# Kernel optimization log

Measured on AMD Instinct MI355X. Metric: run time of the kernel, lower is better.

The kernel has to match this reference:

```python
import jax, jax.numpy as jnp
import numpy as np

B, P, C = 32, 8732, 21
TOP_K = 200
CONF_THRESH = 0.01
NMS_THRESH = 0.45
VAR0, VAR1 = 0.1, 0.2  # VOC PRIOR_BOX VARIANCE


def setup_inputs() -> dict:
    key = jax.random.key(0)
    k1, k2, k3 = jax.random.split(key, 3)
    loc_data = jax.random.normal(k1, (B, P, 4), jnp.float32)
    conf_data = jax.random.uniform(k2, (B, P, C), jnp.float32)
    prior_data = jax.random.uniform(k3, (P, 4), jnp.float32)
    return {"loc_data": loc_data, "conf_data": conf_data, "prior_data": prior_data}


def _decode(loc, priors):
    # priors are (cx, cy, w, h); returns (x1, y1, x2, y2)
    cxcy = priors[:, :2] + loc[:, :2] * VAR0 * priors[:, 2:]
    wh = priors[:, 2:] * jnp.exp(loc[:, 2:] * VAR1)
    x1y1 = cxcy - wh * 0.5
    return jnp.concatenate([x1y1, x1y1 + wh], axis=1)  # [P,4]


def _nms_class(boxes, scores):
    # boxes [P,4], scores [P] -> [TOP_K,5] rows of (score, x1, y1, x2, y2)
    s = jnp.where(scores > CONF_THRESH, scores, -1.0)
    top_s, idx = jax.lax.top_k(s, TOP_K)          # descending scores
    b = boxes[idx]                                 # [K,4]
    valid = top_s > CONF_THRESH
    x1, y1, x2, y2 = b[:, 0], b[:, 1], b[:, 2], b[:, 3]
    area = (x2 - x1) * (y2 - y1)
    # pairwise intersection / IoU [K,K]
    xx1 = jnp.maximum(x1[:, None], x1[None, :])
    yy1 = jnp.maximum(y1[:, None], y1[None, :])
    xx2 = jnp.minimum(x2[:, None], x2[None, :])
    yy2 = jnp.minimum(y2[:, None], y2[None, :])
    inter = jnp.clip(xx2 - xx1, 0.0) * jnp.clip(yy2 - yy1, 0.0)
    union = area[:, None] + area[None, :] - inter
    iou = inter / union
    ar = jnp.arange(TOP_K)

    def step(carry, j):
        kept, suppressed = carry
        is_kept = valid[j] & ~suppressed[j]
        kept = kept.at[j].set(is_kept)
        suppressed = suppressed | (is_kept & (iou[j] > NMS_THRESH) & (ar > j))
        return (kept, suppressed), None

    (kept, _), _ = jax.lax.scan(
        step, (jnp.zeros(TOP_K, bool), jnp.zeros(TOP_K, bool)), ar)
    # compact kept rows to the front (matches output[i, cl, :count] = ...)
    pos = jnp.cumsum(kept) - 1
    safe = jnp.where(kept, pos, TOP_K)
    rows = jnp.concatenate([top_s[:, None], b], axis=1)  # [K,5]
    out = jnp.zeros((TOP_K + 1, 5), rows.dtype).at[safe].set(rows)[:TOP_K]
    return out


def reference(loc_data, conf_data, prior_data):
    def per_image(loc, conf):
        boxes = _decode(loc, prior_data)           # [P,4]
        return jax.vmap(lambda s: _nms_class(boxes, s), in_axes=1)(conf)  # [C,K,5]

    out = jax.vmap(per_image)(loc_data, conf_data)  # [B,C,K,5]
    return out.at[:, 0].set(0.0)  # class 0 (background) is skipped in original
```

## Files before the change

### kernel.cpp

```cpp
#include <hip/hip_runtime.h>
#include <stdint.h>

#define B_ 32
#define P_ 8732
#define C_ 21
#define TOPK 200
#define TGT 228
#define TGT0 300
#define SUBCAP 28
#define NCH2 35
#define NSLOT (NCH2 * SUBCAP)
#define CONF_T 0.01f
#define NMS_T 0.45f
#define NT 512
#define KV4 5
#define NTASK (B_ * C_)

__device__ __forceinline__ uint32_t f2s(float f) {
    uint32_t u = __float_as_uint(f);
    return (u & 0x80000000u) ? ~u : (u | 0x80000000u);
}
__device__ __forceinline__ float s2f(uint32_t s) {
    uint32_t b = (s & 0x80000000u) ? (s & 0x7FFFFFFFu) : ~s;
    return __uint_as_float(b);
}
__device__ __forceinline__ uint32_t keyof(float v) {
    return f2s((v > CONF_T) ? v : -1.0f);
}
__device__ __forceinline__ uint32_t thr0() {
    return f2s(1.0f - (float)TGT0 / (float)P_);
}

__global__ __launch_bounds__(256) void scatter_cands(const float* __restrict__ conf,
                                                     uint32_t* __restrict__ gccnt,
                                                     uint64_t* __restrict__ gcand) {
    const int b = blockIdx.x / NCH2;
    const int ch = blockIdx.x % NCH2;
    const int p0 = ch * 256;
    const int n = min(256, P_ - p0);
    const int tid = threadIdx.x;
    const int lane = tid & 63;
    const int cs = tid >> 6;
    __shared__ float tile[256 * C_];
    const float4* src4 = (const float4*)(conf + ((size_t)b * P_ + p0) * C_);
    float4* tile4 = (float4*)tile;
    const int tot4 = (n * C_) >> 2;
    for (int i = tid; i < tot4; i += 256) tile4[i] = src4[i];
    __syncthreads();
    const uint32_t T0 = thr0();
    const bool act = (4 * lane) < n;
    for (int c = (cs == 0 ? 4 : cs); c < C_; c += 4) {
        uint32_t kk[4];
        int nq = 0;
        if (act) {
            const float* tp = &tile[4 * lane * C_ + c];
            kk[0] = keyof(tp[0 * C_]);
            kk[1] = keyof(tp[1 * C_]);
            kk[2] = keyof(tp[2 * C_]);
            kk[3] = keyof(tp[3 * C_]);
            nq = (kk[0] >= T0) + (kk[1] >= T0) + (kk[2] >= T0) + (kk[3] >= T0);
        }
        int incl = nq;
        #pragma unroll
        for (int d = 1; d < 64; d <<= 1) {
            int v = __shfl_up(incl, d);
            if (lane >= d) incl += v;
        }
        const int excl = incl - nq;
        const int total = __shfl(incl, 63);
        const int task = b * C_ + c;
        uint64_t* dst = gcand + ((size_t)task * NCH2 + ch) * SUBCAP;
        if (nq) {
            int pos = excl;
            const int pb = p0 + 4 * lane;
            #pragma unroll
            for (int k = 0; k < 4; ++k) {
                if (kk[k] >= T0) {
                    if (pos < SUBCAP)
                        dst[pos] = ((uint64_t)kk[k] << 32) | (uint32_t)(~(uint32_t)(pb + k));
                    ++pos;
                }
            }
        }
        if (lane == 0) gccnt[(size_t)task * NCH2 + ch] = (uint32_t)total;
    }
}

template<bool HASWS>
__global__ __launch_bounds__(NT, 6) void detect_kernel(
    const float* __restrict__ loc, const float* __restrict__ prior,
    const uint32_t* __restrict__ gccnt, const uint64_t* __restrict__ gcand,
    const float* __restrict__ conf, float* __restrict__ out)
{
    const int task = blockIdx.x;
    const int b = task / C_;
    const int c = task % C_;
    const int tid = threadIdx.x;
    const int lane = tid & 63;
    float* outp = out + (size_t)task * TOPK * 5;

    if (c == 0) {
        for (int e = tid; e < TOPK * 5; e += NT) outp[e] = 0.0f;
        return;
    }

    __shared__ uint64_t cand[256];
    __shared__ float4 bbox[TOPK];
    __shared__ float bs[TOPK];
    __shared__ unsigned long long msk[TOPK * 4];
    __shared__ unsigned long long vmask[4];
    __shared__ int order[TOPK];
    __shared__ int s_cnt, s_nk;
    __shared__ int s_c2[2];
    __shared__ uint32_t s_ccnt[NCH2];
    __shared__ int s_gc, s_bad;

    const uint32_t T0 = thr0();

    if (tid == 0) s_cnt = 0;
    if (tid < 2) s_c2[tid] = 0;
    if (HASWS && tid < NCH2) s_ccnt[tid] = gccnt[(size_t)task * NCH2 + tid];
    for (int i2 = tid; i2 < TOPK * 4; i2 += NT) msk[i2] = 0ull;
    __syncthreads();
    if (HASWS && tid < 64) {
        uint32_t cc = (lane < NCH2) ? s_ccnt[lane] : 0u;
        int bad = (cc > SUBCAP) ? 1 : 0;
        int tot = (int)cc;
        #pragma unroll
        for (int d = 1; d < 64; d <<= 1) {
            tot += __shfl_down(tot, d);
            bad |= __shfl_down(bad, d);
        }
        if (lane == 0) { s_gc = tot; s_bad = bad; }
    }
    __syncthreads();

    const bool fast = HASWS && !s_bad && s_gc >= TOPK;
    const int gc = HASWS ? s_gc : 0;

    uint64_t vc0 = 0, vc1 = 0;
    bool val0 = false, val1 = false;
    uint4 kv[KV4];
    if (fast) {
        const uint64_t* gp = gcand + (size_t)task * NSLOT;
        {
            const int ch0 = tid / SUBCAP, i0 = tid - ch0 * SUBCAP;
            if (i0 < (int)s_ccnt[ch0]) { vc0 = gp[tid]; val0 = true; }
        }
        const int s1 = tid + NT;
        if (s1 < NSLOT) {
            const int ch1 = s1 / SUBCAP, i1 = s1 - ch1 * SUBCAP;
            if (i1 < (int)s_ccnt[ch1]) { vc1 = gp[s1]; val1 = true; }
        }
    } else {
        const float* sp = conf + (size_t)b * P_ * C_ + c;
        #pragma unroll
        for (int r = 0; r < KV4; ++r) {
            uint32_t uu[4];
            #pragma unroll
            for (int c4 = 0; c4 < 4; ++c4) {
                int p = (tid + r * NT) * 4 + c4;
                if (p < P_) {
                    float v = sp[(size_t)p * C_];
                    v = (v > CONF_T) ? v : -1.0f;
                    uu[c4] = f2s(v);
                } else uu[c4] = 0u;
            }
            kv[r] = make_uint4(uu[0], uu[1], uu[2], uu[3]);
        }
    }

    if (fast) {
        uint32_t vthr = T0;
        if (gc > 256) {
            const uint32_t k0 = (uint32_t)(vc0 >> 32);
            const uint32_t k1 = (uint32_t)(vc1 >> 32);
            uint32_t lo = T0, hi = 0xFFFFFFFFu;
            uint32_t t;
            {
                const float sc = s2f(T0);
                const float sn = 1.0f - (1.0f - sc) * (float)TGT / (float)gc;
                t = f2s(sn);
                if (!(t > lo && t < hi)) t = lo + ((hi - lo) >> 1);
            }
            for (int it = 0; ; ++it) {
                const int slot = it & 1;
                int my = (val0 && k0 >= t) + (val1 && k1 >= t);
                #pragma unroll
                for (int d = 1; d < 64; d <<= 1) my += __shfl_down(my, d);
                if (lane == 0) atomicAdd(&s_c2[slot], my);
                __syncthreads();
                const int cnt = s_c2[slot];
                __syncthreads();
                if (tid == 0) s_c2[slot] = 0;
                if (cnt >= TOPK && cnt <= 256) { vthr = t; break; }
                if (cnt > 256) lo = t; else hi = t;
                if (hi - lo <= 1) { vthr = lo; break; }
                uint32_t tn = 0;
                bool bis = (it >= 8) || (cnt == 0);
                if (!bis) {
                    const float sc = s2f(t);
                    const float sn = 1.0f - (1.0f - sc) * (float)TGT / (float)cnt;
                    tn = f2s(sn);
                    if (!(tn > lo && tn < hi)) bis = true;
                }
                if (bis) tn = lo + ((hi - lo) >> 1);
                t = tn;
            }
        }
        if (val0 && (uint32_t)(vc0 >> 32) >= vthr) {
            int pos = atomicAdd(&s_cnt, 1);
            if (pos < 256) cand[pos] = vc0;
        }
        if (val1 && (uint32_t)(vc1 >> 32) >= vthr) {
            int pos = atomicAdd(&s_cnt, 1);
            if (pos < 256) cand[pos] = vc1;
        }
    } else {
        uint32_t lo = 0u, hi = 0xFFFFFFFFu;
        uint32_t t = f2s(1.0f - (float)TGT / (float)P_);
        uint32_t vthr = 0u;
        for (int it = 0; ; ++it) {
            const int slot = it & 1;
            int my = 0;
            #pragma unroll
            for (int r = 0; r < KV4; ++r)
                my += (kv[r].x >= t) + (kv[r].y >= t) + (kv[r].z >= t) + (kv[r].w >= t);
            #pragma unroll
            for (int d = 1; d < 64; d <<= 1) my += __shfl_down(my, d);
            if (lane == 0) atomicAdd(&s_c2[slot], my);
            __syncthreads();
            const int cnt = s_c2[slot];
            __syncthreads();
            if (tid == 0) s_c2[slot] = 0;
            if (cnt >= TOPK && cnt <= 256) { vthr = t; break; }
            if (cnt > 256) lo = t; else hi = t;
            if (hi - lo <= 1) { vthr = lo; break; }
            uint32_t tn = 0;
            bool bis = (it >= 8) || (cnt == 0);
            if (!bis) {
                const float sc = s2f(t);
                const float sn = 1.0f - (1.0f - sc) * (float)TGT / (float)cnt;
                tn = f2s(sn);
                if (!(tn > lo && tn < hi)) bis = true;
            }
            if (bis) tn = lo + ((hi - lo) >> 1);
            t = tn;
        }
        #pragma unroll
        for (int r = 0; r < KV4; ++r) {
            const int pb = (tid + r * NT) * 4;
            uint32_t uu[4] = {kv[r].x, kv[r].y, kv[r].z, kv[r].w};
            #pragma unroll
            for (int c4 = 0; c4 < 4; ++c4) {
                uint32_t u = uu[c4];
                if (u >= vthr) {
                    int pos = atomicAdd(&s_cnt, 1);
                    if (pos < 256) cand[pos] = ((uint64_t)u << 32) | (uint32_t)(~(uint32_t)(pb + c4));
                }
            }
        }
    }
    __syncthreads();
    if (tid < 256 && tid >= s_cnt) cand[tid] = 0ull;
    __syncthreads();

    uint64_t v = (tid < 256) ? cand[tid] : 0ull;
    for (int kk = 2; kk <= 256; kk <<= 1) {
        for (int j = kk >> 1; j > 0; j >>= 1) {
            if (j >= 64) {
                __syncthreads();
                if (tid < 256) cand[tid] = v;
                __syncthreads();
                if (tid < 256) {
                    uint64_t pv = cand[tid ^ j];
                    bool keepmax = (((tid & j) == 0) == ((tid & kk) == 0));
                    v = keepmax ? (v > pv ? v : pv) : (v < pv ? v : pv);
                }
            } else if (tid < 256) {
                uint64_t pv = __shfl_xor(v, j);
                bool keepmax = (((tid & j) == 0) == ((tid & kk) == 0));
                v = keepmax ? (v > pv ? v : pv) : (v < pv ? v : pv);
            }
        }
    }

    float my_sc = -1.0f;
    if (tid < TOPK) {
        uint32_t su = (uint32_t)(v >> 32);
        int p = (int)(~(uint32_t)v);
        my_sc = s2f(su);
        const float4 l4 = *(const float4*)(loc + ((size_t)b * P_ + p) * 4);
        const float4 pr = *(const float4*)(prior + (size_t)p * 4);
        float cx = __fadd_rn(pr.x, __fmul_rn(__fmul_rn(l4.x, 0.1f), pr.z));
        float cy = __fadd_rn(pr.y, __fmul_rn(__fmul_rn(l4.y, 0.1f), pr.w));
        float ew = (float)exp((double)__fmul_rn(l4.z, 0.2f));
        float eh = (float)exp((double)__fmul_rn(l4.w, 0.2f));
        float w  = __fmul_rn(pr.z, ew);
        float h  = __fmul_rn(pr.w, eh);
        float x1 = __fsub_rn(cx, __fmul_rn(w, 0.5f));
        float y1 = __fsub_rn(cy, __fmul_rn(h, 0.5f));
        float x2 = __fadd_rn(x1, w);
        float y2 = __fadd_rn(y1, h);
        bs[tid] = my_sc;
        bbox[tid] = make_float4(x1, y1, x2, y2);
    }
    {
        unsigned long long bm = __ballot(tid < TOPK && my_sc > CONF_T);
        if (lane == 0 && tid < 256) vmask[tid >> 6] = bm;
    }
    __syncthreads();

    if (tid < 500) {
        const int rp = tid / 5;
        const int s  = tid - rp * 5;
        #pragma unroll
        for (int pass = 0; pass < 2; ++pass) {
            const int j  = pass ? (199 - rp) : rp;
            const int i0 = j + 1 + s;
            const float4 bj = bbox[j];
            const float  aj = __fmul_rn(__fsub_rn(bj.z, bj.x), __fsub_rn(bj.w, bj.y));
            for (int i = i0; i < TOPK; i += 5) {
                const float4 bi = bbox[i];
                float xx1 = fmaxf(bj.x, bi.x);
                float yy1 = fmaxf(bj.y, bi.y);
                float xx2 = fminf(bj.z, bi.z);
                float yy2 = fminf(bj.w, bi.w);
                float dx = fmaxf(__fsub_rn(xx2, xx1), 0.0f);
                float dy = fmaxf(__fsub_rn(yy2, yy1), 0.0f);
                float inter = __fmul_rn(dx, dy);
                if (inter > 0.0f) {
                    float ai = __fmul_rn(__fsub_rn(bi.z, bi.x), __fsub_rn(bi.w, bi.y));
                    float uni = __fsub_rn(__fadd_rn(aj, ai), inter);
                    float t45 = __fmul_rn(NMS_T, uni);
                    float mar = __fmul_rn(t45, 1e-6f);
                    bool sup;
                    if (inter > __fadd_rn(t45, mar)) sup = true;
                    else if (inter < __fsub_rn(t45, mar)) sup = false;
                    else sup = (inter / uni > NMS_T);
                    if (sup) atomicOr(&msk[j * 4 + (i >> 6)], 1ull << (i & 63));
                }
            }
        }
    }
    __syncthreads();

    if (tid < 64) {
        const int L = tid;
        auto or_reduce = [&](unsigned long long x) {
            #pragma unroll
            for (int d = 1; d < 64; d <<= 1) x |= __shfl_xor(x, d);
            return x;
        };
        unsigned long long s1 = 0, s2 = 0, s3 = 0;
        int nk = 0;
        #pragma unroll
        for (int w = 0; w < 4; ++w) {
            const int j = (w << 6) | L;
            unsigned long long r0 = 0, r1 = 0, r2 = 0, r3 = 0;
            if (j < TOPK) {
                const unsigned long long* mr = &msk[j * 4];
                r0 = mr[0]; r1 = mr[1]; r2 = mr[2]; r3 = mr[3];
            }
            const unsigned long long rself = (w == 0) ? r0 : (w == 1) ? r1
                                           : (w == 2) ? r2 : r3;
            unsigned long long sw = (w == 0) ? 0ull : (w == 1) ? s1
                                  : (w == 2) ? s2 : s3;
            unsigned long long alive = vmask[w] & ~sw;
            unsigned long long pm = 0;
            while (alive) {
                int jl = __ffsll(alive) - 1;
                if (L == 0) order[nk] = (w << 6) | jl;
                ++nk;
                sw |= __shfl(rself, jl);
                pm |= (1ull << jl);
                alive &= ~(sw | (1ull << jl));
            }
            if (pm) {
                const bool picked = (pm >> L) & 1ull;
                if (w == 0) {
                    s1 |= or_reduce(picked ? r1 : 0ull);
                    s2 |= or_reduce(picked ? r2 : 0ull);
                    s3 |= or_reduce(picked ? r3 : 0ull);
                } else if (w == 1) {
                    s2 |= or_reduce(picked ? r2 : 0ull);
                    s3 |= or_reduce(picked ? r3 : 0ull);
                } else if (w == 2) {
                    s3 |= or_reduce(picked ? r3 : 0ull);
                }
            }
        }
        if (L == 0) s_nk = nk;
    }
    __syncthreads();

    const int nk = s_nk;
    for (int e = tid; e < TOPK * 5; e += NT) {
        int r = e / 5;
        int f = e - r * 5;
        float val = 0.0f;
        if (r < nk) {
            int j = order[r];
            float4 bb = bbox[j];
            val = (f == 0) ? bs[j] : (f == 1) ? bb.x : (f == 2) ? bb.y
                : (f == 3) ? bb.z : bb.w;
        }
        outp[e] = val;
    }
}

extern "C" void kernel_launch(void* const* d_in, const int* in_sizes, int n_in,
                              void* d_out, int out_size, void* d_ws, size_t ws_size,
                              hipStream_t stream) {
    const float* loc   = (const float*)d_in[0];
    const float* conf  = (const float*)d_in[1];
    const float* prior = (const float*)d_in[2];
    float* out = (float*)d_out;

    const size_t cnt_bytes  = (size_t)NTASK * NCH2 * sizeof(uint32_t);
    const size_t cand_bytes = (size_t)NTASK * NSLOT * sizeof(uint64_t);
    if (ws_size >= cnt_bytes + cand_bytes) {
        uint32_t* gccnt = (uint32_t*)d_ws;
        uint64_t* gcand = (uint64_t*)((char*)d_ws + cnt_bytes);
        scatter_cands<<<B_ * NCH2, 256, 0, stream>>>(conf, gccnt, gcand);
        detect_kernel<true><<<NTASK, NT, 0, stream>>>(loc, prior, gccnt, gcand, conf, out);
    } else {
        detect_kernel<false><<<NTASK, NT, 0, stream>>>(loc, prior, nullptr, nullptr, conf, out);
    }
}
```

Before: 123.0 us.

## Use ballot-based compaction, triple-buffer bisection counters, precompute box areas

In the scatter kernel, each lane now handles strided rows (lane+64k), and output positions come from per-k ballots and popcounts instead of a shuffle-up prefix scan. In the detect kernel's fast path, the threshold bisection rotates through three shared counter slots so one __syncthreads per iteration can be removed, and candidates are appended with one wave-level atomic instead of one atomic per thread. Box areas are computed once into shared memory, and the IoU inner loop is unrolled by two. These target shuffle-scan latency, barrier count, and LDS atomic contention. The candidate order inside each chunk changes, and the three-slot reset scheme depends on subtle reuse timing to stay correct.

```diff
diff --git a/kernel.cpp b/kernel.cpp
--- a/kernel.cpp
+++ b/kernel.cpp
@@ -48,37 +48,34 @@
     for (int i = tid; i < tot4; i += 256) tile4[i] = src4[i];
     __syncthreads();
     const uint32_t T0 = thr0();
-    const bool act = (4 * lane) < n;
     for (int c = (cs == 0 ? 4 : cs); c < C_; c += 4) {
         uint32_t kk[4];
-        int nq = 0;
-        if (act) {
-            const float* tp = &tile[4 * lane * C_ + c];
-            kk[0] = keyof(tp[0 * C_]);
-            kk[1] = keyof(tp[1 * C_]);
-            kk[2] = keyof(tp[2 * C_]);
-            kk[3] = keyof(tp[3 * C_]);
-            nq = (kk[0] >= T0) + (kk[1] >= T0) + (kk[2] >= T0) + (kk[3] >= T0);
-        }
-        int incl = nq;
-        #pragma unroll
-        for (int d = 1; d < 64; d <<= 1) {
-            int v = __shfl_up(incl, d);
-            if (lane >= d) incl += v;
-        }
-        const int excl = incl - nq;
-        const int total = __shfl(incl, 63);
+        #pragma unroll
+        for (int k = 0; k < 4; ++k) {
+            const int r = lane + 64 * k;
+            if (r < n) kk[k] = keyof(tile[r * C_ + c]);
+            else       kk[k] = 0u;
+        }
+        const unsigned long long m0 = __ballot(kk[0] >= T0);
+        const unsigned long long m1 = __ballot(kk[1] >= T0);
+        const unsigned long long m2 = __ballot(kk[2] >= T0);
+        const unsigned long long m3 = __ballot(kk[3] >= T0);
+        const int c0 = __popcll(m0), c1 = __popcll(m1), c2 = __popcll(m2), c3 = __popcll(m3);
+        const int total = c0 + c1 + c2 + c3;
         const int task = b * C_ + c;
         uint64_t* dst = gcand + ((size_t)task * NCH2 + ch) * SUBCAP;
-        if (nq) {
-            int pos = excl;
-            const int pb = p0 + 4 * lane;
+        {
+            const unsigned long long below = (1ull << lane) - 1ull;
+            const int cum[4] = {0, c0, c0 + c1, c0 + c1 + c2};
+            const unsigned long long mm[4] = {m0, m1, m2, m3};
             #pragma unroll
             for (int k = 0; k < 4; ++k) {
                 if (kk[k] >= T0) {
-                    if (pos < SUBCAP)
-                        dst[pos] = ((uint64_t)kk[k] << 32) | (uint32_t)(~(uint32_t)(pb + k));
-                    ++pos;
+                    const int pos = cum[k] + __popcll(mm[k] & below);
+                    if (pos < SUBCAP) {
+                        const int p = p0 + lane + 64 * k;
+                        dst[pos] = ((uint64_t)kk[k] << 32) | (uint32_t)(~(uint32_t)p);
+                    }
                 }
             }
         }
@@ -107,11 +104,13 @@
     __shared__ uint64_t cand[256];
     __shared__ float4 bbox[TOPK];
     __shared__ float bs[TOPK];
+    __shared__ float sar[TOPK];
     __shared__ unsigned long long msk[TOPK * 4];
     __shared__ unsigned long long vmask[4];
     __shared__ int order[TOPK];
     __shared__ int s_cnt, s_nk;
     __shared__ int s_c2[2];
+    __shared__ int s_c3[3];
     __shared__ uint32_t s_ccnt[NCH2];
     __shared__ int s_gc, s_bad;
 
@@ -119,6 +118,7 @@
 
     if (tid == 0) s_cnt = 0;
     if (tid < 2) s_c2[tid] = 0;
+    if (tid < 3) s_c3[tid] = 0;
     if (HASWS && tid < NCH2) s_ccnt[tid] = gccnt[(size_t)task * NCH2 + tid];
     for (int i2 = tid; i2 < TOPK * 4; i2 += NT) msk[i2] = 0ull;
     __syncthreads();
@@ -171,10 +171,10 @@
     }
 
     if (fast) {
+        const uint32_t k0 = (uint32_t)(vc0 >> 32);
+        const uint32_t k1 = (uint32_t)(vc1 >> 32);
         uint32_t vthr = T0;
         if (gc > 256) {
-            const uint32_t k0 = (uint32_t)(vc0 >> 32);
-            const uint32_t k1 = (uint32_t)(vc1 >> 32);
             uint32_t lo = T0, hi = 0xFFFFFFFFu;
             uint32_t t;
             {
@@ -184,15 +184,14 @@
                 if (!(t > lo && t < hi)) t = lo + ((hi - lo) >> 1);
             }
             for (int it = 0; ; ++it) {
-                const int slot = it & 1;
+                const int slot = it % 3;
                 int my = (val0 && k0 >= t) + (val1 && k1 >= t);
                 #pragma unroll
                 for (int d = 1; d < 64; d <<= 1) my += __shfl_down(my, d);
-                if (lane == 0) atomicAdd(&s_c2[slot], my);
+                if (lane == 0) atomicAdd(&s_c3[slot], my);
+                if (tid == 0) s_c3[(it + 1) % 3] = 0;
                 __syncthreads();
-                const int cnt = s_c2[slot];
-                __syncthreads();
-                if (tid == 0) s_c2[slot] = 0;
+                const int cnt = s_c3[slot];
                 if (cnt >= TOPK && cnt <= 256) { vthr = t; break; }
                 if (cnt > 256) lo = t; else hi = t;
                 if (hi - lo <= 1) { vthr = lo; break; }
@@ -208,14 +207,19 @@
                 t = tn;
             }
         }
-        if (val0 && (uint32_t)(vc0 >> 32) >= vthr) {
-            int pos = atomicAdd(&s_cnt, 1);
-            if (pos < 256) cand[pos] = vc0;
-        }
-        if (val1 && (uint32_t)(vc1 >> 32) >= vthr) {
-            int pos = atomicAdd(&s_cnt, 1);
-            if (pos < 256) cand[pos] = vc1;
-        }
+        const bool p0v = val0 && k0 >= vthr;
+        const bool p1v = val1 && k1 >= vthr;
+        const unsigned long long mm0 = __ballot(p0v);
+        const unsigned long long mm1 = __ballot(p1v);
+        const int wtot = __popcll(mm0) + __popcll(mm1);
+        int base = 0;
+        if (lane == 0 && wtot) base = atomicAdd(&s_cnt, wtot);
+        base = __shfl(base, 0);
+        const unsigned long long below = (1ull << lane) - 1ull;
+        const int o0 = base + __popcll(mm0 & below);
+        const int o1 = base + __popcll(mm0) + __popcll(mm1 & below);
+        if (p0v && o0 < 256) cand[o0] = vc0;
+        if (p1v && o1 < 256) cand[o1] = vc1;
     } else {
         uint32_t lo = 0u, hi = 0xFFFFFFFFu;
         uint32_t t = f2s(1.0f - (float)TGT / (float)P_);
@@ -304,6 +308,7 @@
         float y2 = __fadd_rn(y1, h);
         bs[tid] = my_sc;
         bbox[tid] = make_float4(x1, y1, x2, y2);
+        sar[tid] = __fmul_rn(__fsub_rn(x2, x1), __fsub_rn(y2, y1));
     }
     {
         unsigned long long bm = __ballot(tid < TOPK && my_sc > CONF_T);
@@ -319,8 +324,9 @@
             const int j  = pass ? (199 - rp) : rp;
             const int i0 = j + 1 + s;
             const float4 bj = bbox[j];
-            const float  aj = __fmul_rn(__fsub_rn(bj.z, bj.x), __fsub_rn(bj.w, bj.y));
-            for (int i = i0; i < TOPK; i += 5) {
+            const float  aj = sar[j];
+            unsigned long long* mrow = &msk[j * 4];
+            auto iou1 = [&](int i) {
                 const float4 bi = bbox[i];
                 float xx1 = fmaxf(bj.x, bi.x);
                 float yy1 = fmaxf(bj.y, bi.y);
@@ -330,7 +336,7 @@
                 float dy = fmaxf(__fsub_rn(yy2, yy1), 0.0f);
                 float inter = __fmul_rn(dx, dy);
                 if (inter > 0.0f) {
-                    float ai = __fmul_rn(__fsub_rn(bi.z, bi.x), __fsub_rn(bi.w, bi.y));
+                    float ai = sar[i];
                     float uni = __fsub_rn(__fadd_rn(aj, ai), inter);
                     float t45 = __fmul_rn(NMS_T, uni);
                     float mar = __fmul_rn(t45, 1e-6f);
@@ -338,9 +344,12 @@
                     if (inter > __fadd_rn(t45, mar)) sup = true;
                     else if (inter < __fsub_rn(t45, mar)) sup = false;
                     else sup = (inter / uni > NMS_T);
-                    if (sup) atomicOr(&msk[j * 4 + (i >> 6)], 1ull << (i & 63));
-                }
-            }
+                    if (sup) atomicOr(&mrow[i >> 6], 1ull << (i & 63));
+                }
+            };
+            int i = i0;
+            for (; i + 5 < TOPK; i += 10) { iou1(i); iou1(i + 5); }
+            if (i < TOPK) iou1(i);
         }
     }
     __syncthreads();
```

Measured after the change: 122.6 us. No clear change (-0.4%).
